# Kernel tuning notes

Measured on AMD Instinct MI355X. Metric: run time of the kernel, lower is better.

Reference implementation:

```python
import jax, jax.numpy as jnp
import numpy as np

HEADS = 16
HEAD_DIM = 4  # attention_channels(64) // num_heads(16)


def setup_inputs() -> dict:
    key = jax.random.key(0)
    ks = jax.random.split(key, 9)
    C, AC = 256, 64
    N, H, W = 1, 64, 64
    s_in = 1.0 / np.sqrt(C)
    s_out = 1.0 / np.sqrt(AC)
    return {
        "X":  jax.random.normal(ks[0], (N, C, H, W), jnp.float32),
        "Wq": jax.random.normal(ks[1], (AC, C), jnp.float32) * s_in,
        "bq": jax.random.normal(ks[2], (AC,), jnp.float32) * 0.01,
        "Wk": jax.random.normal(ks[3], (AC, C), jnp.float32) * s_in,
        "bk": jax.random.normal(ks[4], (AC,), jnp.float32) * 0.01,
        "Wv": jax.random.normal(ks[5], (AC, C), jnp.float32) * s_in,
        "bv": jax.random.normal(ks[6], (AC,), jnp.float32) * 0.01,
        "Wo": jax.random.normal(ks[7], (C, AC), jnp.float32) * s_out,
        "bo": jax.random.normal(ks[8], (C,), jnp.float32) * 0.01,
    }


def _l2norm_over_dim(x, eps=1e-12):
    # torch F.normalize(dim=-2): x / max(||x||_2, eps) along head-dim axis
    n = jnp.sqrt(jnp.sum(x * x, axis=-2, keepdims=True))
    return x / jnp.maximum(n, eps)


def reference(X, Wq, bq, Wk, bk, Wv, bv, Wo, bo):
    N, C, H, W = X.shape
    L = H * W
    def proj(Wm, bm):
        # 1x1 conv == channel matmul; reshape to (N, heads, d, L)
        y = jnp.einsum('oc,nchw->nohw', Wm, X) + bm[None, :, None, None]
        return y.reshape(N, HEADS, HEAD_DIM, L)
    Q = _l2norm_over_dim(proj(Wq, bq))
    K = _l2norm_over_dim(proj(Wk, bk))
    V = proj(Wv, bv)
    # attention_weights[l, m] = q_l . k_m, softmax over m (rows)
    A = jax.nn.softmax(jnp.einsum('nhdl,nhdm->nhlm', Q, K), axis=-1)
    # faithful to original: out = V @ A  -> out[d, i] = sum_j V[d, j] * A[j, i]
    out = jnp.einsum('nhdj,nhji->nhdi', V, A)
    out = out.reshape(N, HEADS * HEAD_DIM, H, W)
    out = jnp.einsum('co,nohw->nchw', Wo, out) + bo[None, :, None, None]
    return out + X
```

## Files before the change

### kernel.cpp

```cpp
#include <hip/hip_runtime.h>
#include <math.h>


constexpr int SL = 4096;
constexpr int NF = 126;

__device__ __forceinline__ float invfact(int e) {
    return e < 2 ? 1.f : e == 2 ? 0.5f : e == 3 ? (1.f / 6.f)
         : e == 4 ? (1.f / 24.f) : (1.f / 120.f);
}
__device__ __forceinline__ void f2abcd(int f, int& A, int& B, int& C, int& D) {
    for (int a = 0; a <= 5; ++a)
        for (int b = 0; b <= 5 - a; ++b)
            for (int c = 0; c <= 5 - a - b; ++c)
                for (int d = 0; d <= 5 - a - b - c; ++d)
                    if (f-- == 0) { A = a; B = b; C = c; D = d; return; }
}

#define FOR_MONOMIALS(BODY)                         \
    {                                               \
        int f = 0;                                  \
        _Pragma("unroll")                           \
        for (int a = 0; a <= 5; ++a)                \
        _Pragma("unroll")                           \
        for (int b = 0; b <= 5 - a; ++b)            \
        _Pragma("unroll")                           \
        for (int c = 0; c <= 5 - a - b; ++c)        \
        _Pragma("unroll")                           \
        for (int d = 0; d <= 5 - a - b - c; ++d) {  \
            BODY;                                   \
            ++f;                                    \
        }                                           \
    }

#define BUILD_POWERS(q)                                   \
    float p0[6], p1[6], p2[6], p3[6];                     \
    p0[0] = p1[0] = p2[0] = p3[0] = 1.f;                  \
    _Pragma("unroll")                                     \
    for (int t_ = 1; t_ < 6; ++t_) {                      \
        p0[t_] = p0[t_ - 1] * (q).x; p1[t_] = p1[t_ - 1] * (q).y; \
        p2[t_] = p2[t_ - 1] * (q).z; p3[t_] = p3[t_ - 1] * (q).w; }

__global__ __launch_bounds__(256) void qkv_kernel(
    const float* __restrict__ X,
    const float* __restrict__ Wq, const float* __restrict__ bq,
    const float* __restrict__ Wk, const float* __restrict__ bk,
    const float* __restrict__ Wv, const float* __restrict__ bv,
    float* __restrict__ Qn, float* __restrict__ Kn, float* __restrict__ V4)
{
    const int tid  = threadIdx.x;
    const int lane = tid & 63;
    const int wv   = __builtin_amdgcn_readfirstlane(tid >> 6);
    const int lt   = blockIdx.x;
    const int rb   = blockIdx.y;
    const int type = rb >> 2;
    const int rit  = (rb & 3) * 16 + wv * 4;
    const int l    = lt * 64 + lane;

    const float* W = type == 0 ? Wq : type == 1 ? Wk : Wv;
    const float* B = type == 0 ? bq : type == 1 ? bk : bv;
    const float* w0 = W + (rit + 0) * 256;
    const float* w1 = W + (rit + 1) * 256;
    const float* w2 = W + (rit + 2) * 256;
    const float* w3 = W + (rit + 3) * 256;

    float y0 = B[rit + 0], y1 = B[rit + 1], y2 = B[rit + 2], y3 = B[rit + 3];
    const float* Xl = X + l;
    #pragma unroll 8
    for (int c = 0; c < 256; ++c) {
        float x = Xl[c * SL];
        y0 = fmaf(w0[c], x, y0);
        y1 = fmaf(w1[c], x, y1);
        y2 = fmaf(w2[c], x, y2);
        y3 = fmaf(w3[c], x, y3);
    }
    if (type < 2) {
        float n = sqrtf(y0*y0 + y1*y1 + y2*y2 + y3*y3);
        float inv = 1.f / fmaxf(n, 1e-12f);
        y0 *= inv; y1 *= inv; y2 *= inv; y3 *= inv;
    }
    const int h = rit >> 2;
    float* base = type == 0 ? Qn : type == 1 ? Kn : V4;
    ((float4*)base)[h * SL + l] = make_float4(y0, y1, y2, y3);
}

template <int FC>
__device__ __forceinline__ void psi_accum(int h, int jc, int tid,
        const float* __restrict__ Kn, float acc[8])
{
    for (int u = 0; u < 4; ++u) {
        int j = jc * 1024 + u * 256 + tid;
        float4 k = ((const float4*)Kn)[h * SL + j];
        BUILD_POWERS(k)
        FOR_MONOMIALS({
            if (f >= FC * 8 && f < FC * 8 + 8)
                acc[f - FC * 8] += (p0[a] * p1[b]) * (p2[c] * p3[d]);
        })
    }
}

__global__ __launch_bounds__(256) void ssum_kernel(
    const float* __restrict__ Kn, float* __restrict__ Sp)
{
    const int tid = threadIdx.x;
    const int fc  = blockIdx.x;
    const int h   = blockIdx.y;
    const int jc  = blockIdx.z;
    float acc[8];
    #pragma unroll
    for (int k = 0; k < 8; ++k) acc[k] = 0.f;
    switch (fc) {
        case 0:  psi_accum<0 >(h, jc, tid, Kn, acc); break;
        case 1:  psi_accum<1 >(h, jc, tid, Kn, acc); break;
        case 2:  psi_accum<2 >(h, jc, tid, Kn, acc); break;
        case 3:  psi_accum<3 >(h, jc, tid, Kn, acc); break;
        case 4:  psi_accum<4 >(h, jc, tid, Kn, acc); break;
        case 5:  psi_accum<5 >(h, jc, tid, Kn, acc); break;
        case 6:  psi_accum<6 >(h, jc, tid, Kn, acc); break;
        case 7:  psi_accum<7 >(h, jc, tid, Kn, acc); break;
        case 8:  psi_accum<8 >(h, jc, tid, Kn, acc); break;
        case 9:  psi_accum<9 >(h, jc, tid, Kn, acc); break;
        case 10: psi_accum<10>(h, jc, tid, Kn, acc); break;
        case 11: psi_accum<11>(h, jc, tid, Kn, acc); break;
        case 12: psi_accum<12>(h, jc, tid, Kn, acc); break;
        case 13: psi_accum<13>(h, jc, tid, Kn, acc); break;
        case 14: psi_accum<14>(h, jc, tid, Kn, acc); break;
        default: psi_accum<15>(h, jc, tid, Kn, acc); break;
    }
    #pragma unroll
    for (int off = 32; off; off >>= 1)
        #pragma unroll
        for (int k = 0; k < 8; ++k) acc[k] += __shfl_down(acc[k], off);
    __shared__ float red[4][8];
    const int lane = tid & 63, wv = tid >> 6;
    if (lane == 0) {
        #pragma unroll
        for (int k = 0; k < 8; ++k) red[wv][k] = acc[k];
    }
    __syncthreads();
    if (tid < 8) {
        int f = fc * 8 + tid;
        if (f < NF) {
            float s = (red[0][tid] + red[1][tid]) + (red[2][tid] + red[3][tid]);
            int A, B, C, D; f2abcd(f, A, B, C, D);
            Sp[(jc * 16 + h) * 128 + f] =
                s * ((invfact(A) * invfact(B)) * (invfact(C) * invfact(D)));
        }
    }
}

__global__ __launch_bounds__(256) void zvz_kernel(
    const float* __restrict__ Qn, const float* __restrict__ Sp,
    const float* __restrict__ V4, float* __restrict__ Vz)
{
    __shared__ float Sf[128];
    const int tid = threadIdx.x;
    const int h   = blockIdx.y;
    if (tid < 128) {
        float s = 0.f;
        #pragma unroll
        for (int jc = 0; jc < 4; ++jc) s += Sp[(jc * 16 + h) * 128 + tid];
        Sf[tid] = s;
    }
    __syncthreads();
    const int j = blockIdx.x * 256 + tid;
    float4 q = ((const float4*)Qn)[h * SL + j];
    BUILD_POWERS(q)
    float z = 0.f;
    FOR_MONOMIALS({ z = fmaf((p0[a]*p1[b])*(p2[c]*p3[d]), Sf[f], z); })
    float inv = 1.f / z;
    float4 v = ((const float4*)V4)[h * SL + j];
    ((float4*)Vz)[h * SL + j] = make_float4(v.x*inv, v.y*inv, v.z*inv, v.w*inv);
}

template <int FC>
__device__ __forceinline__ void m_accum(int h, int jc, int tid,
        const float* __restrict__ Qn, const float* __restrict__ Vz,
        float acc[32])
{
    for (int u = 0; u < 8; ++u) {
        int j = jc * 2048 + u * 256 + tid;
        float4 q = ((const float4*)Qn)[h * SL + j];
        float4 v = ((const float4*)Vz)[h * SL + j];
        BUILD_POWERS(q)
        FOR_MONOMIALS({
            if (f >= FC * 8 && f < FC * 8 + 8) {
                const int fi = f - FC * 8;
                float m = (p0[a] * p1[b]) * (p2[c] * p3[d]);
                acc[fi*4+0] = fmaf(m, v.x, acc[fi*4+0]);
                acc[fi*4+1] = fmaf(m, v.y, acc[fi*4+1]);
                acc[fi*4+2] = fmaf(m, v.z, acc[fi*4+2]);
                acc[fi*4+3] = fmaf(m, v.w, acc[fi*4+3]);
            }
        })
    }
}

__global__ __launch_bounds__(256) void mmat_kernel(
    const float* __restrict__ Qn, const float* __restrict__ Vz,
    float* __restrict__ Mp)
{
    const int tid = threadIdx.x;
    const int fc  = blockIdx.x;
    const int h   = blockIdx.y;
    const int jc  = blockIdx.z;
    float acc[32];
    #pragma unroll
    for (int k = 0; k < 32; ++k) acc[k] = 0.f;
    switch (fc) {
        case 0:  m_accum<0 >(h, jc, tid, Qn, Vz, acc); break;
        case 1:  m_accum<1 >(h, jc, tid, Qn, Vz, acc); break;
        case 2:  m_accum<2 >(h, jc, tid, Qn, Vz, acc); break;
        case 3:  m_accum<3 >(h, jc, tid, Qn, Vz, acc); break;
        case 4:  m_accum<4 >(h, jc, tid, Qn, Vz, acc); break;
        case 5:  m_accum<5 >(h, jc, tid, Qn, Vz, acc); break;
        case 6:  m_accum<6 >(h, jc, tid, Qn, Vz, acc); break;
        case 7:  m_accum<7 >(h, jc, tid, Qn, Vz, acc); break;
        case 8:  m_accum<8 >(h, jc, tid, Qn, Vz, acc); break;
        case 9:  m_accum<9 >(h, jc, tid, Qn, Vz, acc); break;
        case 10: m_accum<10>(h, jc, tid, Qn, Vz, acc); break;
        case 11: m_accum<11>(h, jc, tid, Qn, Vz, acc); break;
        case 12: m_accum<12>(h, jc, tid, Qn, Vz, acc); break;
        case 13: m_accum<13>(h, jc, tid, Qn, Vz, acc); break;
        case 14: m_accum<14>(h, jc, tid, Qn, Vz, acc); break;
        default: m_accum<15>(h, jc, tid, Qn, Vz, acc); break;
    }
    #pragma unroll
    for (int off = 32; off; off >>= 1)
        #pragma unroll
        for (int k = 0; k < 32; ++k) acc[k] += __shfl_down(acc[k], off);
    __shared__ float red[4][32];
    const int lane = tid & 63, wv = tid >> 6;
    if (lane == 0) {
        #pragma unroll
        for (int k = 0; k < 32; ++k) red[wv][k] = acc[k];
    }
    __syncthreads();
    if (tid < 32) {
        int fi = tid >> 2, dd = tid & 3;
        int f = fc * 8 + fi;
        if (f < NF) {
            float s = (red[0][tid] + red[1][tid]) + (red[2][tid] + red[3][tid]);
            int A, B, C, D; f2abcd(f, A, B, C, D);
            s *= (invfact(A) * invfact(B)) * (invfact(C) * invfact(D));
            Mp[((jc * 16 + h) * 128 + f) * 4 + dd] = s;
        }
    }
}

__global__ __launch_bounds__(256) void outfuse_kernel(
    const float* __restrict__ Kn, const float* __restrict__ Mp,
    const float* __restrict__ Wo, const float* __restrict__ bo,
    const float* __restrict__ X, float* __restrict__ Y)
{
    __shared__ __align__(16) float ML[16 * 128 * 4];
    __shared__ float AOL[64 * 33];
    const int tid = threadIdx.x;
    const int it  = blockIdx.x;
    const int cb  = blockIdx.y;
    const int i0  = it * 32;

    {
        const float4* Mp4 = (const float4*)Mp;
        float4* ML4 = (float4*)ML;
        #pragma unroll
        for (int w = 0; w < 8; ++w) {
            int e = tid + w * 256;
            float4 a = Mp4[e], b = Mp4[2048 + e];
            ML4[e] = make_float4(a.x+b.x, a.y+b.y, a.z+b.z, a.w+b.w);
        }
    }
    __syncthreads();

    #pragma unroll
    for (int r = 0; r < 2; ++r) {
        int p = tid + r * 256;
        int pos = p & 31, h = p >> 5;
        float4 k = ((const float4*)Kn)[h * SL + i0 + pos];
        BUILD_POWERS(k)
        const float4* Mh = ((const float4*)ML) + h * 128;
        float a0 = 0.f, a1 = 0.f, a2 = 0.f, a3 = 0.f;
        FOR_MONOMIALS({
            float m = (p0[a] * p1[b]) * (p2[c] * p3[d]);
            float4 mm = Mh[f];
            a0 = fmaf(m, mm.x, a0); a1 = fmaf(m, mm.y, a1);
            a2 = fmaf(m, mm.z, a2); a3 = fmaf(m, mm.w, a3);
        })
        AOL[(h * 4 + 0) * 33 + pos] = a0;
        AOL[(h * 4 + 1) * 33 + pos] = a1;
        AOL[(h * 4 + 2) * 33 + pos] = a2;
        AOL[(h * 4 + 3) * 33 + pos] = a3;
    }
    __syncthreads();

    const int pos = tid & 31, cg = tid >> 5;
    const int chb = cb * 64 + cg * 8;
    float acc[8];
    #pragma unroll
    for (int u = 0; u < 8; ++u) acc[u] = 0.f;
    #pragma unroll 4
    for (int ob = 0; ob < 16; ++ob) {
        float x0 = AOL[(ob * 4 + 0) * 33 + pos];
        float x1 = AOL[(ob * 4 + 1) * 33 + pos];
        float x2 = AOL[(ob * 4 + 2) * 33 + pos];
        float x3 = AOL[(ob * 4 + 3) * 33 + pos];
        #pragma unroll
        for (int u = 0; u < 8; ++u) {
            float4 w4 = ((const float4*)Wo)[(chb + u) * 16 + ob];
            acc[u] = fmaf(w4.x, x0, fmaf(w4.y, x1,
                     fmaf(w4.z, x2, fmaf(w4.w, x3, acc[u]))));
        }
    }
    #pragma unroll
    for (int u = 0; u < 8; ++u) {
        int ch = chb + u;
        Y[ch * SL + i0 + pos] = acc[u] + bo[ch] + X[ch * SL + i0 + pos];
    }
}

extern "C" void kernel_launch(void* const* d_in, const int* in_sizes, int n_in,
                              void* d_out, int out_size, void* d_ws, size_t ws_size,
                              hipStream_t stream)
{
    const float* X  = (const float*)d_in[0];
    const float* Wq = (const float*)d_in[1];
    const float* bq = (const float*)d_in[2];
    const float* Wk = (const float*)d_in[3];
    const float* bk = (const float*)d_in[4];
    const float* Wv = (const float*)d_in[5];
    const float* bv = (const float*)d_in[6];
    const float* Wo = (const float*)d_in[7];
    const float* bo = (const float*)d_in[8];
    float* Y = (float*)d_out;

    char* w = (char*)d_ws;
    float* Qn = (float*)(w + (0 << 20));
    float* Kn = (float*)(w + (1 << 20));
    float* V4 = (float*)(w + (2 << 20));
    float* Vz = (float*)(w + (3 << 20));
    float* Sp = (float*)(w + (4 << 20));
    float* Mp = (float*)(w + (4 << 20) + (128 << 10));

    qkv_kernel<<<dim3(64, 12), 256, 0, stream>>>(X, Wq, bq, Wk, bk, Wv, bv,
                                                 Qn, Kn, V4);
    ssum_kernel<<<dim3(16, 16, 4), 256, 0, stream>>>(Kn, Sp);
    zvz_kernel<<<dim3(16, 16), 256, 0, stream>>>(Qn, Sp, V4, Vz);
    mmat_kernel<<<dim3(16, 16, 2), 256, 0, stream>>>(Qn, Vz, Mp);
    outfuse_kernel<<<dim3(128, 4), 256, 0, stream>>>(Kn, Mp, Wo, bo, X, Y);
}
```

Before: 121.9 us.

## Fuse five attention kernels into one cooperative persistent kernel with grid syncs

Folds the QKV projection, key-feature sum, normalizer, M-matrix accumulation and output projection into one cooperative kernel with 1024 blocks separated by grid-wide barriers. A small fold phase pre-reduces the two M partials into a compact 126-entry-per-head buffer, and the normalizer phase spreads the 126 monomials across four waves with an LDS reduction. This aims to remove per-launch overhead and inter-kernel gaps, at the cost of idle blocks in phases with fewer work items, grid-sync overhead, and a larger shared-memory footprint that may limit occupancy. A fallback of separate kernels remains for when four blocks per CU cannot be resident.

```diff
diff --git a/kernel.cpp b/kernel.cpp
--- a/kernel.cpp
+++ b/kernel.cpp
@@ -1,6 +1,9 @@
 #include <hip/hip_runtime.h>
+#include <hip/hip_cooperative_groups.h>
 #include <math.h>
 
+
+namespace cg = cooperative_groups;
 
 constexpr int SL = 4096;
 constexpr int NF = 126;
@@ -41,18 +44,19 @@
         p0[t_] = p0[t_ - 1] * (q).x; p1[t_] = p1[t_ - 1] * (q).y; \
         p2[t_] = p2[t_ - 1] * (q).z; p3[t_] = p3[t_ - 1] * (q).w; }
 
-__global__ __launch_bounds__(256) void qkv_kernel(
+
+__device__ __forceinline__ void phase_qkv(int bid, int tid,
     const float* __restrict__ X,
     const float* __restrict__ Wq, const float* __restrict__ bq,
     const float* __restrict__ Wk, const float* __restrict__ bk,
     const float* __restrict__ Wv, const float* __restrict__ bv,
-    float* __restrict__ Qn, float* __restrict__ Kn, float* __restrict__ V4)
-{
-    const int tid  = threadIdx.x;
+    float* __restrict__ Qn, float* __restrict__ Kn, float* __restrict__ V4f)
+{
+    if (bid >= 768) return;
     const int lane = tid & 63;
     const int wv   = __builtin_amdgcn_readfirstlane(tid >> 6);
-    const int lt   = blockIdx.x;
-    const int rb   = blockIdx.y;
+    const int lt   = bid & 63;
+    const int rb   = bid >> 6;
     const int type = rb >> 2;
     const int rit  = (rb & 3) * 16 + wv * 4;
     const int l    = lt * 64 + lane;
@@ -80,7 +84,7 @@
         y0 *= inv; y1 *= inv; y2 *= inv; y3 *= inv;
     }
     const int h = rit >> 2;
-    float* base = type == 0 ? Qn : type == 1 ? Kn : V4;
+    float* base = type == 0 ? Qn : type == 1 ? Kn : V4f;
     ((float4*)base)[h * SL + l] = make_float4(y0, y1, y2, y3);
 }
 
@@ -99,13 +103,10 @@
     }
 }
 
-__global__ __launch_bounds__(256) void ssum_kernel(
+__device__ __forceinline__ void phase_ssum(int bid, int tid, float* lds,
     const float* __restrict__ Kn, float* __restrict__ Sp)
 {
-    const int tid = threadIdx.x;
-    const int fc  = blockIdx.x;
-    const int h   = blockIdx.y;
-    const int jc  = blockIdx.z;
+    const int fc = bid & 15, h = (bid >> 4) & 15, jc = bid >> 8;
     float acc[8];
     #pragma unroll
     for (int k = 0; k < 8; ++k) acc[k] = 0.f;
@@ -131,46 +132,72 @@
     for (int off = 32; off; off >>= 1)
         #pragma unroll
         for (int k = 0; k < 8; ++k) acc[k] += __shfl_down(acc[k], off);
-    __shared__ float red[4][8];
+    float* red = lds;
     const int lane = tid & 63, wv = tid >> 6;
     if (lane == 0) {
         #pragma unroll
-        for (int k = 0; k < 8; ++k) red[wv][k] = acc[k];
+        for (int k = 0; k < 8; ++k) red[wv * 8 + k] = acc[k];
     }
     __syncthreads();
     if (tid < 8) {
         int f = fc * 8 + tid;
         if (f < NF) {
-            float s = (red[0][tid] + red[1][tid]) + (red[2][tid] + red[3][tid]);
+            float s = (red[tid] + red[8 + tid]) + (red[16 + tid] + red[24 + tid]);
             int A, B, C, D; f2abcd(f, A, B, C, D);
             Sp[(jc * 16 + h) * 128 + f] =
                 s * ((invfact(A) * invfact(B)) * (invfact(C) * invfact(D)));
         }
     }
-}
-
-__global__ __launch_bounds__(256) void zvz_kernel(
+    __syncthreads();
+}
+
+template <int W>
+__device__ __forceinline__ float z_part(const float p0[6], const float p1[6],
+        const float p2[6], const float p3[6], const float* Sf)
+{
+    float z = 0.f;
+    FOR_MONOMIALS({
+        if (f >= W * 32 && f < W * 32 + 32)
+            z = fmaf((p0[a] * p1[b]) * (p2[c] * p3[d]), Sf[f], z);
+    })
+    return z;
+}
+
+__device__ __forceinline__ void phase_zvz(int bid, int tid, float* lds,
     const float* __restrict__ Qn, const float* __restrict__ Sp,
-    const float* __restrict__ V4, float* __restrict__ Vz)
-{
-    __shared__ float Sf[128];
-    const int tid = threadIdx.x;
-    const int h   = blockIdx.y;
+    const float* __restrict__ V4f, float* __restrict__ Vz)
+{
+    float* SfL = lds;
+    float* ZQ  = lds + 128;
+    const int h = bid & 15, jt = bid >> 4;
     if (tid < 128) {
         float s = 0.f;
         #pragma unroll
         for (int jc = 0; jc < 4; ++jc) s += Sp[(jc * 16 + h) * 128 + tid];
-        Sf[tid] = s;
-    }
-    __syncthreads();
-    const int j = blockIdx.x * 256 + tid;
+        SfL[tid] = s;
+    }
+    __syncthreads();
+    const int j = jt * 64 + (tid & 63);
+    const int w = tid >> 6;
     float4 q = ((const float4*)Qn)[h * SL + j];
     BUILD_POWERS(q)
-    float z = 0.f;
-    FOR_MONOMIALS({ z = fmaf((p0[a]*p1[b])*(p2[c]*p3[d]), Sf[f], z); })
-    float inv = 1.f / z;
-    float4 v = ((const float4*)V4)[h * SL + j];
-    ((float4*)Vz)[h * SL + j] = make_float4(v.x*inv, v.y*inv, v.z*inv, v.w*inv);
+    float z;
+    switch (w) {
+        case 0:  z = z_part<0>(p0, p1, p2, p3, SfL); break;
+        case 1:  z = z_part<1>(p0, p1, p2, p3, SfL); break;
+        case 2:  z = z_part<2>(p0, p1, p2, p3, SfL); break;
+        default: z = z_part<3>(p0, p1, p2, p3, SfL); break;
+    }
+    ZQ[tid] = z;
+    __syncthreads();
+    if (tid < 64) {
+        float zt = (ZQ[tid] + ZQ[64 + tid]) + (ZQ[128 + tid] + ZQ[192 + tid]);
+        float inv = 1.f / zt;
+        float4 v = ((const float4*)V4f)[h * SL + jt * 64 + tid];
+        ((float4*)Vz)[h * SL + jt * 64 + tid] =
+            make_float4(v.x * inv, v.y * inv, v.z * inv, v.w * inv);
+    }
+    __syncthreads();
 }
 
 template <int FC>
@@ -196,14 +223,12 @@
     }
 }
 
-__global__ __launch_bounds__(256) void mmat_kernel(
+__device__ __forceinline__ void phase_mmat(int bid, int tid, float* lds,
     const float* __restrict__ Qn, const float* __restrict__ Vz,
     float* __restrict__ Mp)
 {
-    const int tid = threadIdx.x;
-    const int fc  = blockIdx.x;
-    const int h   = blockIdx.y;
-    const int jc  = blockIdx.z;
+    if (bid >= 512) return;
+    const int fc = bid & 15, h = (bid >> 4) & 15, jc = bid >> 8;
     float acc[32];
     #pragma unroll
     for (int k = 0; k < 32; ++k) acc[k] = 0.f;
@@ -229,56 +254,63 @@
     for (int off = 32; off; off >>= 1)
         #pragma unroll
         for (int k = 0; k < 32; ++k) acc[k] += __shfl_down(acc[k], off);
-    __shared__ float red[4][32];
+    float* red = lds;
     const int lane = tid & 63, wv = tid >> 6;
     if (lane == 0) {
         #pragma unroll
-        for (int k = 0; k < 32; ++k) red[wv][k] = acc[k];
+        for (int k = 0; k < 32; ++k) red[wv * 32 + k] = acc[k];
     }
     __syncthreads();
     if (tid < 32) {
         int fi = tid >> 2, dd = tid & 3;
         int f = fc * 8 + fi;
         if (f < NF) {
-            float s = (red[0][tid] + red[1][tid]) + (red[2][tid] + red[3][tid]);
+            float s = (red[tid] + red[32 + tid]) + (red[64 + tid] + red[96 + tid]);
             int A, B, C, D; f2abcd(f, A, B, C, D);
             s *= (invfact(A) * invfact(B)) * (invfact(C) * invfact(D));
             Mp[((jc * 16 + h) * 128 + f) * 4 + dd] = s;
         }
     }
-}
-
-__global__ __launch_bounds__(256) void outfuse_kernel(
-    const float* __restrict__ Kn, const float* __restrict__ Mp,
+    __syncthreads();
+}
+
+__device__ __forceinline__ void phase_fold(int bid, int tid,
+    const float* __restrict__ Mp, float* __restrict__ Mf)
+{
+    if (bid >= 32) return;
+    int ed = bid * 256 + tid;
+    if (ed < 8064) {
+        int h = ed / 504;
+        int r = ed - h * 504;
+        int src = h * 512 + r;
+        Mf[ed] = Mp[src] + Mp[8192 + src];
+    }
+}
+
+__device__ __forceinline__ void phase_out(int bid, int tid, float* lds,
+    const float* __restrict__ Kn, const float* __restrict__ Mf,
     const float* __restrict__ Wo, const float* __restrict__ bo,
     const float* __restrict__ X, float* __restrict__ Y)
 {
-    __shared__ __align__(16) float ML[16 * 128 * 4];
-    __shared__ float AOL[64 * 33];
-    const int tid = threadIdx.x;
-    const int it  = blockIdx.x;
-    const int cb  = blockIdx.y;
-    const int i0  = it * 32;
-
-    {
-        const float4* Mp4 = (const float4*)Mp;
-        float4* ML4 = (float4*)ML;
-        #pragma unroll
-        for (int w = 0; w < 8; ++w) {
-            int e = tid + w * 256;
-            float4 a = Mp4[e], b = Mp4[2048 + e];
-            ML4[e] = make_float4(a.x+b.x, a.y+b.y, a.z+b.z, a.w+b.w);
-        }
-    }
-    __syncthreads();
-
+    if (bid >= 512) return;
+    float4* ML4 = (float4*)lds;
+    float*  AOL = lds + 8064;
+    const int it = bid & 127, cb = bid >> 7;
+    const int i0 = it * 32;
+    const float4* Mf4 = (const float4*)Mf;
+    #pragma unroll
+    for (int w = 0; w < 8; ++w) {
+        int e = tid + w * 256;
+        if (e < 2016) ML4[e] = Mf4[e];
+    }
+    __syncthreads();
     #pragma unroll
     for (int r = 0; r < 2; ++r) {
         int p = tid + r * 256;
         int pos = p & 31, h = p >> 5;
         float4 k = ((const float4*)Kn)[h * SL + i0 + pos];
         BUILD_POWERS(k)
-        const float4* Mh = ((const float4*)ML) + h * 128;
+        const float4* Mh = ML4 + h * 126;
         float a0 = 0.f, a1 = 0.f, a2 = 0.f, a3 = 0.f;
         FOR_MONOMIALS({
             float m = (p0[a] * p1[b]) * (p2[c] * p3[d]);
@@ -292,9 +324,8 @@
         AOL[(h * 4 + 3) * 33 + pos] = a3;
     }
     __syncthreads();
-
-    const int pos = tid & 31, cg = tid >> 5;
-    const int chb = cb * 64 + cg * 8;
+    const int pos = tid & 31, cg_ = tid >> 5;
+    const int chb = cb * 64 + cg_ * 8;
     float acc[8];
     #pragma unroll
     for (int u = 0; u < 8; ++u) acc[u] = 0.f;
@@ -316,6 +347,62 @@
         int ch = chb + u;
         Y[ch * SL + i0 + pos] = acc[u] + bo[ch] + X[ch * SL + i0 + pos];
     }
+}
+
+
+__global__ __launch_bounds__(256, 4) void mega_kernel(
+    const float* __restrict__ X,
+    const float* __restrict__ Wq, const float* __restrict__ bq,
+    const float* __restrict__ Wk, const float* __restrict__ bk,
+    const float* __restrict__ Wv, const float* __restrict__ bv,
+    const float* __restrict__ Wo, const float* __restrict__ bo,
+    float* __restrict__ Y,
+    float* __restrict__ Qn, float* __restrict__ Kn,
+    float* __restrict__ V4f, float* __restrict__ Vz,
+    float* __restrict__ Sp, float* __restrict__ Mp, float* __restrict__ Mf)
+{
+    __shared__ __align__(16) float lds[10176];
+    cg::grid_group g = cg::this_grid();
+    const int bid = blockIdx.x, tid = threadIdx.x;
+    phase_qkv(bid, tid, X, Wq, bq, Wk, bk, Wv, bv, Qn, Kn, V4f);
+    g.sync();
+    phase_ssum(bid, tid, lds, Kn, Sp);
+    g.sync();
+    phase_zvz(bid, tid, lds, Qn, Sp, V4f, Vz);
+    g.sync();
+    phase_mmat(bid, tid, lds, Qn, Vz, Mp);
+    g.sync();
+    phase_fold(bid, tid, Mp, Mf);
+    g.sync();
+    phase_out(bid, tid, lds, Kn, Mf, Wo, bo, X, Y);
+}
+
+__global__ __launch_bounds__(256) void k_qkv(
+    const float* X, const float* Wq, const float* bq, const float* Wk,
+    const float* bk, const float* Wv, const float* bv,
+    float* Qn, float* Kn, float* V4f)
+{ phase_qkv(blockIdx.x, threadIdx.x, X, Wq, bq, Wk, bk, Wv, bv, Qn, Kn, V4f); }
+
+__global__ __launch_bounds__(256) void k_ssum(const float* Kn, float* Sp)
+{ __shared__ float lds[32]; phase_ssum(blockIdx.x, threadIdx.x, lds, Kn, Sp); }
+
+__global__ __launch_bounds__(256) void k_zvz(
+    const float* Qn, const float* Sp, const float* V4f, float* Vz)
+{ __shared__ float lds[384]; phase_zvz(blockIdx.x, threadIdx.x, lds, Qn, Sp, V4f, Vz); }
+
+__global__ __launch_bounds__(256) void k_mmat(
+    const float* Qn, const float* Vz, float* Mp)
+{ __shared__ float lds[128]; phase_mmat(blockIdx.x, threadIdx.x, lds, Qn, Vz, Mp); }
+
+__global__ __launch_bounds__(256) void k_fold(const float* Mp, float* Mf)
+{ phase_fold(blockIdx.x, threadIdx.x, Mp, Mf); }
+
+__global__ __launch_bounds__(256) void k_out(
+    const float* Kn, const float* Mf, const float* Wo, const float* bo,
+    const float* X, float* Y)
+{
+    __shared__ __align__(16) float lds[10176];
+    phase_out(blockIdx.x, threadIdx.x, lds, Kn, Mf, Wo, bo, X, Y);
 }
 
 extern "C" void kernel_launch(void* const* d_in, const int* in_sizes, int n_in,
@@ -334,17 +421,31 @@
     float* Y = (float*)d_out;
 
     char* w = (char*)d_ws;
-    float* Qn = (float*)(w + (0 << 20));
-    float* Kn = (float*)(w + (1 << 20));
-    float* V4 = (float*)(w + (2 << 20));
-    float* Vz = (float*)(w + (3 << 20));
-    float* Sp = (float*)(w + (4 << 20));
-    float* Mp = (float*)(w + (4 << 20) + (128 << 10));
-
-    qkv_kernel<<<dim3(64, 12), 256, 0, stream>>>(X, Wq, bq, Wk, bk, Wv, bv,
-                                                 Qn, Kn, V4);
-    ssum_kernel<<<dim3(16, 16, 4), 256, 0, stream>>>(Kn, Sp);
-    zvz_kernel<<<dim3(16, 16), 256, 0, stream>>>(Qn, Sp, V4, Vz);
-    mmat_kernel<<<dim3(16, 16, 2), 256, 0, stream>>>(Qn, Vz, Mp);
-    outfuse_kernel<<<dim3(128, 4), 256, 0, stream>>>(Kn, Mp, Wo, bo, X, Y);
-}
+    float* Qn  = (float*)(w + (0 << 20));
+    float* Kn  = (float*)(w + (1 << 20));
+    float* V4f = (float*)(w + (2 << 20));
+    float* Vz  = (float*)(w + (3 << 20));
+    float* Sp  = (float*)(w + (4 << 20));
+    float* Mp  = (float*)(w + (4 << 20) + (128 << 10));
+    float* Mf  = (float*)(w + (4 << 20) + (256 << 10));
+
+    int maxb = 0;
+    hipError_t qe = hipOccupancyMaxActiveBlocksPerMultiprocessor(
+        &maxb, mega_kernel, 256, 0);
+    if (qe == hipSuccess && maxb >= 4) {
+        void* args[] = { (void*)&X, (void*)&Wq, (void*)&bq, (void*)&Wk,
+                         (void*)&bk, (void*)&Wv, (void*)&bv, (void*)&Wo,
+                         (void*)&bo, (void*)&Y, (void*)&Qn, (void*)&Kn,
+                         (void*)&V4f, (void*)&Vz, (void*)&Sp, (void*)&Mp,
+                         (void*)&Mf };
+        (void)hipLaunchCooperativeKernel((const void*)mega_kernel,
+                                         dim3(1024), dim3(256), args, 0, stream);
+    } else {
+        k_qkv <<<768,  256, 0, stream>>>(X, Wq, bq, Wk, bk, Wv, bv, Qn, Kn, V4f);
+        k_ssum<<<1024, 256, 0, stream>>>(Kn, Sp);
+        k_zvz <<<1024, 256, 0, stream>>>(Qn, Sp, V4f, Vz);
+        k_mmat<<<512,  256, 0, stream>>>(Qn, Vz, Mp);
+        k_fold<<<32,   256, 0, stream>>>(Mp, Mf);
+        k_out <<<512,  256, 0, stream>>>(Kn, Mf, Wo, bo, X, Y);
+    }
+}
```

New measurement: 126.1 us. +3.4%, slower.

## Fuse normalizer computation into moment accumulation kernel, drop Vz buffer

Applied to the files above, without the earlier changes.

Merges the zvz kernel, which computed the per-position softmax normalizer and wrote scaled V, into the moment-accumulation kernel. Each block now recomputes the normalizer z from all 126 monomials and accumulates 16 monomials instead of 8, over 4 sequence chunks. This removes one launch and the Vz global round trip. In exchange, the normalizer work is repeated once per feature chunk (8 times), register pressure grows with 64 accumulators, and outfuse must sum 4 partials instead of 2.

```diff
diff --git a/kernel.cpp b/kernel.cpp
--- a/kernel.cpp
+++ b/kernel.cpp
@@ -149,96 +149,81 @@
     }
 }
 
-__global__ __launch_bounds__(256) void zvz_kernel(
-    const float* __restrict__ Qn, const float* __restrict__ Sp,
-    const float* __restrict__ V4, float* __restrict__ Vz)
+template <int FC>
+__device__ __forceinline__ void zm_accum(int h, int jc, int tid,
+        const float* __restrict__ Qn, const float* __restrict__ V4,
+        const float* __restrict__ Sf, float acc[64])
+{
+    for (int u = 0; u < 4; ++u) {
+        int j = jc * 1024 + u * 256 + tid;
+        float4 q = ((const float4*)Qn)[h * SL + j];
+        BUILD_POWERS(q)
+        float z = 0.f;
+        float mchunk[16];
+        FOR_MONOMIALS({
+            float mono = (p0[a] * p1[b]) * (p2[c] * p3[d]);
+            z = fmaf(mono, Sf[f], z);
+            if (f >= FC * 16 && f < FC * 16 + 16) mchunk[f - FC * 16] = mono;
+        })
+        float inv = 1.f / z;
+        float4 v = ((const float4*)V4)[h * SL + j];
+        float vx = v.x * inv, vy = v.y * inv, vz_ = v.z * inv, vw = v.w * inv;
+        #pragma unroll
+        for (int fi = 0; fi < 16; ++fi) {
+            float m = mchunk[fi];
+            acc[fi*4+0] = fmaf(m, vx,  acc[fi*4+0]);
+            acc[fi*4+1] = fmaf(m, vy,  acc[fi*4+1]);
+            acc[fi*4+2] = fmaf(m, vz_, acc[fi*4+2]);
+            acc[fi*4+3] = fmaf(m, vw,  acc[fi*4+3]);
+        }
+    }
+}
+
+__global__ __launch_bounds__(256) void zmv_kernel(
+    const float* __restrict__ Qn, const float* __restrict__ V4,
+    const float* __restrict__ Sp, float* __restrict__ Mp)
 {
     __shared__ float Sf[128];
-    const int tid = threadIdx.x;
-    const int h   = blockIdx.y;
-    if (tid < 128) {
-        float s = 0.f;
-        #pragma unroll
-        for (int jc = 0; jc < 4; ++jc) s += Sp[(jc * 16 + h) * 128 + tid];
-        Sf[tid] = s;
-    }
-    __syncthreads();
-    const int j = blockIdx.x * 256 + tid;
-    float4 q = ((const float4*)Qn)[h * SL + j];
-    BUILD_POWERS(q)
-    float z = 0.f;
-    FOR_MONOMIALS({ z = fmaf((p0[a]*p1[b])*(p2[c]*p3[d]), Sf[f], z); })
-    float inv = 1.f / z;
-    float4 v = ((const float4*)V4)[h * SL + j];
-    ((float4*)Vz)[h * SL + j] = make_float4(v.x*inv, v.y*inv, v.z*inv, v.w*inv);
-}
-
-template <int FC>
-__device__ __forceinline__ void m_accum(int h, int jc, int tid,
-        const float* __restrict__ Qn, const float* __restrict__ Vz,
-        float acc[32])
-{
-    for (int u = 0; u < 8; ++u) {
-        int j = jc * 2048 + u * 256 + tid;
-        float4 q = ((const float4*)Qn)[h * SL + j];
-        float4 v = ((const float4*)Vz)[h * SL + j];
-        BUILD_POWERS(q)
-        FOR_MONOMIALS({
-            if (f >= FC * 8 && f < FC * 8 + 8) {
-                const int fi = f - FC * 8;
-                float m = (p0[a] * p1[b]) * (p2[c] * p3[d]);
-                acc[fi*4+0] = fmaf(m, v.x, acc[fi*4+0]);
-                acc[fi*4+1] = fmaf(m, v.y, acc[fi*4+1]);
-                acc[fi*4+2] = fmaf(m, v.z, acc[fi*4+2]);
-                acc[fi*4+3] = fmaf(m, v.w, acc[fi*4+3]);
-            }
-        })
-    }
-}
-
-__global__ __launch_bounds__(256) void mmat_kernel(
-    const float* __restrict__ Qn, const float* __restrict__ Vz,
-    float* __restrict__ Mp)
-{
+    __shared__ float red[4][64];
     const int tid = threadIdx.x;
     const int fc  = blockIdx.x;
     const int h   = blockIdx.y;
     const int jc  = blockIdx.z;
-    float acc[32];
-    #pragma unroll
-    for (int k = 0; k < 32; ++k) acc[k] = 0.f;
+
+    if (tid < 128) {
+        float s = 0.f;
+        #pragma unroll
+        for (int p = 0; p < 4; ++p) s += Sp[(p * 16 + h) * 128 + tid];
+        Sf[tid] = s;
+    }
+    __syncthreads();
+
+    float acc[64];
+    #pragma unroll
+    for (int k = 0; k < 64; ++k) acc[k] = 0.f;
     switch (fc) {
-        case 0:  m_accum<0 >(h, jc, tid, Qn, Vz, acc); break;
-        case 1:  m_accum<1 >(h, jc, tid, Qn, Vz, acc); break;
-        case 2:  m_accum<2 >(h, jc, tid, Qn, Vz, acc); break;
-        case 3:  m_accum<3 >(h, jc, tid, Qn, Vz, acc); break;
-        case 4:  m_accum<4 >(h, jc, tid, Qn, Vz, acc); break;
-        case 5:  m_accum<5 >(h, jc, tid, Qn, Vz, acc); break;
-        case 6:  m_accum<6 >(h, jc, tid, Qn, Vz, acc); break;
-        case 7:  m_accum<7 >(h, jc, tid, Qn, Vz, acc); break;
-        case 8:  m_accum<8 >(h, jc, tid, Qn, Vz, acc); break;
-        case 9:  m_accum<9 >(h, jc, tid, Qn, Vz, acc); break;
-        case 10: m_accum<10>(h, jc, tid, Qn, Vz, acc); break;
-        case 11: m_accum<11>(h, jc, tid, Qn, Vz, acc); break;
-        case 12: m_accum<12>(h, jc, tid, Qn, Vz, acc); break;
-        case 13: m_accum<13>(h, jc, tid, Qn, Vz, acc); break;
-        case 14: m_accum<14>(h, jc, tid, Qn, Vz, acc); break;
-        default: m_accum<15>(h, jc, tid, Qn, Vz, acc); break;
+        case 0:  zm_accum<0>(h, jc, tid, Qn, V4, Sf, acc); break;
+        case 1:  zm_accum<1>(h, jc, tid, Qn, V4, Sf, acc); break;
+        case 2:  zm_accum<2>(h, jc, tid, Qn, V4, Sf, acc); break;
+        case 3:  zm_accum<3>(h, jc, tid, Qn, V4, Sf, acc); break;
+        case 4:  zm_accum<4>(h, jc, tid, Qn, V4, Sf, acc); break;
+        case 5:  zm_accum<5>(h, jc, tid, Qn, V4, Sf, acc); break;
+        case 6:  zm_accum<6>(h, jc, tid, Qn, V4, Sf, acc); break;
+        default: zm_accum<7>(h, jc, tid, Qn, V4, Sf, acc); break;
     }
     #pragma unroll
     for (int off = 32; off; off >>= 1)
         #pragma unroll
-        for (int k = 0; k < 32; ++k) acc[k] += __shfl_down(acc[k], off);
-    __shared__ float red[4][32];
+        for (int k = 0; k < 64; ++k) acc[k] += __shfl_down(acc[k], off);
     const int lane = tid & 63, wv = tid >> 6;
     if (lane == 0) {
         #pragma unroll
-        for (int k = 0; k < 32; ++k) red[wv][k] = acc[k];
-    }
-    __syncthreads();
-    if (tid < 32) {
+        for (int k = 0; k < 64; ++k) red[wv][k] = acc[k];
+    }
+    __syncthreads();
+    if (tid < 64) {
         int fi = tid >> 2, dd = tid & 3;
-        int f = fc * 8 + fi;
+        int f = fc * 16 + fi;
         if (f < NF) {
             float s = (red[0][tid] + red[1][tid]) + (red[2][tid] + red[3][tid]);
             int A, B, C, D; f2abcd(f, A, B, C, D);
@@ -266,8 +251,10 @@
         #pragma unroll
         for (int w = 0; w < 8; ++w) {
             int e = tid + w * 256;
-            float4 a = Mp4[e], b = Mp4[2048 + e];
-            ML4[e] = make_float4(a.x+b.x, a.y+b.y, a.z+b.z, a.w+b.w);
+            float4 a = Mp4[e],        b = Mp4[2048 + e];
+            float4 c = Mp4[4096 + e], d = Mp4[6144 + e];
+            ML4[e] = make_float4((a.x+b.x)+(c.x+d.x), (a.y+b.y)+(c.y+d.y),
+                                 (a.z+b.z)+(c.z+d.z), (a.w+b.w)+(c.w+d.w));
         }
     }
     __syncthreads();
@@ -337,14 +324,12 @@
     float* Qn = (float*)(w + (0 << 20));
     float* Kn = (float*)(w + (1 << 20));
     float* V4 = (float*)(w + (2 << 20));
-    float* Vz = (float*)(w + (3 << 20));
-    float* Sp = (float*)(w + (4 << 20));
-    float* Mp = (float*)(w + (4 << 20) + (128 << 10));
+    float* Sp = (float*)(w + (3 << 20));
+    float* Mp = (float*)(w + (3 << 20) + (128 << 10));
 
     qkv_kernel<<<dim3(64, 12), 256, 0, stream>>>(X, Wq, bq, Wk, bk, Wv, bv,
                                                  Qn, Kn, V4);
     ssum_kernel<<<dim3(16, 16, 4), 256, 0, stream>>>(Kn, Sp);
-    zvz_kernel<<<dim3(16, 16), 256, 0, stream>>>(Qn, Sp, V4, Vz);
-    mmat_kernel<<<dim3(16, 16, 2), 256, 0, stream>>>(Qn, Vz, Mp);
+    zmv_kernel<<<dim3(8, 16, 4), 256, 0, stream>>>(Qn, V4, Sp, Mp);
     outfuse_kernel<<<dim3(128, 4), 256, 0, stream>>>(Kn, Mp, Wo, bo, X, Y);
 }
```

Result: slower. 135.6 us (+11.2%).
